# Kernel tuning notes

Measured on AMD Instinct MI355X. Metric: run time of the kernel, lower is better.

Reference implementation:

```python
import jax, jax.numpy as jnp
import numpy as np
import math

HIDDEN = 256
D = 256  # attention_head_size (num_heads=1)
LN_EPS = 1e-5


def setup_inputs() -> dict:
    key = jax.random.key(0)
    ks = jax.random.split(key, 12)
    b, n = 8, 256
    s = 0.02
    return {
        "hidden_states": jax.random.normal(ks[0], (b, n, HIDDEN), jnp.float32),
        "structure_matrix": jax.random.normal(ks[1], (b, n, n, D), jnp.float32),
        "Wq": jax.random.normal(ks[2], (HIDDEN, D), jnp.float32) * s,
        "bq": jnp.zeros((D,), jnp.float32),
        "Wk": jax.random.normal(ks[3], (D, D), jnp.float32) * s,
        "bk": jnp.zeros((D,), jnp.float32),
        "Wv": jax.random.normal(ks[4], (HIDDEN, D), jnp.float32) * s,
        "bv": jnp.zeros((D,), jnp.float32),
        "Wo": jax.random.normal(ks[5], (D, D), jnp.float32) * s,
        "bo": jnp.zeros((D,), jnp.float32),
        "ln_gamma": jnp.ones((D,), jnp.float32),
        "ln_beta": jnp.zeros((D,), jnp.float32),
    }


def _layer_norm(x, gamma, beta):
    mu = jnp.mean(x, axis=-1, keepdims=True)
    var = jnp.mean(jnp.square(x - mu), axis=-1, keepdims=True)
    return (x - mu) * jax.lax.rsqrt(var + LN_EPS) * gamma + beta


def reference(hidden_states, structure_matrix, Wq, bq, Wk, bk, Wv, bv, Wo, bo, ln_gamma, ln_beta):
    # projections
    q = hidden_states @ Wq + bq            # [b, n, d]
    k = structure_matrix @ Wk + bk         # [b, l, r, d]
    v = hidden_states @ Wv + bv            # [b, n, d]
    # pair-biased attention: each (l, r) pair attends over all n tokens
    scores = jnp.einsum('bnd,blrd->blrn', q, k) / math.sqrt(D)  # [b, l, r, n]
    probs = jax.nn.softmax(scores, axis=-1)  # dropout is identity in eval
    ctx = jnp.einsum('blrn,bnd->blrd', probs, v)  # [b, l, r, d]
    out = ctx @ Wo + bo
    return _layer_norm(out + structure_matrix, ln_gamma, ln_beta)
```

## Files before the change

kernel.cpp:

```cpp
#include <hip/hip_runtime.h>
#include <hip/hip_bf16.h>

typedef __attribute__((ext_vector_type(8))) short short8v;
typedef __attribute__((ext_vector_type(4))) float f32x4;
typedef __attribute__((ext_vector_type(8))) unsigned short us8;
typedef const __attribute__((address_space(1))) void* gas_t;
typedef __attribute__((address_space(3))) void* las_t;

__device__ __forceinline__ unsigned short f2bf(float f) {
  union { __hip_bfloat16 h; unsigned short u; } c;
  c.h = __float2bfloat16(f);
  return c.u;
}
__device__ __forceinline__ unsigned int f2bf2(float lo, float hi) {
  union { __hip_bfloat162 h; unsigned int u; } c;
  c.h = __float22bfloat162_rn(make_float2(lo, hi));
  return c.u;
}

__global__ __launch_bounds__(256) void tr_wk(const float* __restrict__ Wk,
                                             float* __restrict__ WkT) {
  __shared__ float sT[64][65];
  const int b = blockIdx.x;
  const int bi = b >> 2, bj = b & 3;
  const int tid = threadIdx.x;
  const int r4 = tid >> 6, c64 = tid & 63;
#pragma unroll
  for (int p = 0; p < 16; p++) {
    const int row = bi * 64 + p * 4 + r4;
    const int col = bj * 64 + c64;
    sT[c64][p * 4 + r4] = Wk[row * 256 + col];
  }
  __syncthreads();
#pragma unroll
  for (int p = 0; p < 16; p++) {
    const int orow = bj * 64 + p * 4 + r4;
    const int ocol = bi * 64 + c64;
    WkT[orow * 256 + ocol] = sT[p * 4 + r4][c64];
  }
}

__global__ __launch_bounds__(256) void make_w(
    const float* __restrict__ WkT, const float* __restrict__ Wq,
    const float* __restrict__ Wv, const float* __restrict__ Wo,
    const float* __restrict__ bq, const float* __restrict__ bk,
    const float* __restrict__ bv, float* __restrict__ WA,
    float* __restrict__ WB, float* __restrict__ wb2,
    float* __restrict__ cq, float* __restrict__ cv, float* __restrict__ cb) {
  __shared__ float wq[256], wv[256], bqs[256], bvs[256];
  const int i = blockIdx.x, t = threadIdx.x;
  wq[t] = Wq[i * 256 + t];
  wv[t] = Wv[i * 256 + t];
  bqs[t] = bq[t];
  bvs[t] = bv[t];
  __syncthreads();
  float sa = 0.f, sb = 0.f;
#pragma unroll 8
  for (int d = 0; d < 256; d++) {
    sa = fmaf(wq[d], WkT[d * 256 + t], sa);
    sb = fmaf(wv[d], Wo[d * 256 + t], sb);
  }
  WA[i * 256 + t] = sa * 0.0625f;
  WB[i * 256 + t] = sb;
  if (t == 0) {
    float s = 0.f;
#pragma unroll 8
    for (int d = 0; d < 256; d++) s = fmaf(wq[d], bk[d], s);
    wb2[i] = s * 0.0625f;
  }
  if (i == 0) {
    float s1 = 0.f, s2 = 0.f;
#pragma unroll 8
    for (int d = 0; d < 256; d++) {
      s1 = fmaf(bqs[d], WkT[d * 256 + t], s1);
      s2 = fmaf(bvs[d], Wo[d * 256 + t], s2);
    }
    cq[t] = s1 * 0.0625f;
    cv[t] = s2;
    if (t == 0) {
      float s = 0.f;
      for (int d = 0; d < 256; d++) s = fmaf(bk[d], bqs[d], s);
      cb[0] = s * 0.0625f;
    }
  }
}

__global__ __launch_bounds__(256) void prep2(
    const float* __restrict__ hs, const float* __restrict__ WA,
    const float* __restrict__ WB, const float* __restrict__ cq,
    const float* __restrict__ cv, const float* __restrict__ wb2,
    const float* __restrict__ cb, unsigned short* __restrict__ W2c,
    unsigned short* __restrict__ V2c, float* __restrict__ bn) {
  __shared__ float rows[8][256];
  __shared__ float w2s[256];
  const int tid = threadIdx.x;
  const int g0 = blockIdx.x * 8;
#pragma unroll
  for (int j = 0; j < 8; j++) rows[j][tid] = hs[(size_t)(g0 + j) * 256 + tid];
  w2s[tid] = wb2[tid];
  __syncthreads();
  const float cqv = cq[tid], cvv = cv[tid];
  float aq[8], av[8];
#pragma unroll
  for (int j = 0; j < 8; j++) { aq[j] = cqv; av[j] = cvv; }
#pragma unroll 8
  for (int i = 0; i < 256; i++) {
    const float wa = WA[i * 256 + tid];
    const float wb = WB[i * 256 + tid];
#pragma unroll
    for (int j = 0; j < 8; j++) {
      aq[j] = fmaf(rows[j][i], wa, aq[j]);
      av[j] = fmaf(rows[j][i], wb, av[j]);
    }
  }
  const int bb = g0 >> 8, n0 = g0 & 255;
  {
    const int kc = tid >> 5, lh = (tid >> 3) & 3, j8 = tid & 7;
    unsigned short* dst = W2c + bb * 65536 + kc * 8192 + (n0 >> 4) * 512 +
                          lh * 128 + (n0 & 15) * 8 + j8;
#pragma unroll
    for (int jj = 0; jj < 8; jj++) dst[jj * 8] = f2bf(aq[jj]);
  }
  {
    const int kc = n0 >> 5, lh = (n0 >> 3) & 3;
    us8 vp;
#pragma unroll
    for (int j = 0; j < 8; j++) vp[j] = f2bf(av[j]);
    *(us8*)(V2c + bb * 65536 + kc * 8192 + (tid >> 4) * 512 + lh * 128 +
            (tid & 15) * 8) = vp;
  }
  if (tid < 8) {
    float s = 0.f;
    for (int i = 0; i < 256; i++) s = fmaf(rows[tid][i], w2s[i], s);
    bn[bb * 256 + n0 + tid] = s + cb[0];
  }
}

__device__ __forceinline__ void stage_b(const unsigned short* src,
                                        unsigned short* lds, int lane) {
#pragma unroll
  for (int i = 0; i < 4; i++)
    __builtin_amdgcn_global_load_lds((gas_t)(src + i * 512 + lane * 8),
                                     (las_t)(lds + i * 512), 16, 0, 0);
}

__global__ __launch_bounds__(256, 3) void pair_attn14(
    const float* __restrict__ S, const float* __restrict__ bo,
    const float* __restrict__ gamma, const float* __restrict__ beta,
    const float* __restrict__ bn, const unsigned short* __restrict__ W2c,
    const unsigned short* __restrict__ V2c, float* __restrict__ out) {
  __shared__ unsigned short sB[3][8192];
  __shared__ float sBn[256];

  const int tid = threadIdx.x;
  const int w = tid >> 6;
  const int lane = tid & 63;
  const int l16 = lane & 15;
  const int lhi = lane >> 4;
  const int bid = blockIdx.x;
  const int idx = (bid & 7) * 1024 + (bid >> 3);
  const int rblk = idx & 3;
  const int lrow = (idx >> 2) & 255;
  const int bat = idx >> 10;

  const size_t base = ((size_t)((bat * 256 + lrow) * 256 + rblk * 64)) * 256;
  const float* Srow = S + base + (size_t)(w * 16 + l16) * 256;

  short8v sf[8];
#pragma unroll
  for (int kc = 0; kc < 8; kc++) {
    const float4 u = *(const float4*)(Srow + kc * 32 + lhi * 8);
    const float4 v = *(const float4*)(Srow + kc * 32 + lhi * 8 + 4);
    us8 p;
    unsigned int* pu = (unsigned int*)&p;
    pu[0] = f2bf2(u.x, u.y);
    pu[1] = f2bf2(u.z, u.w);
    pu[2] = f2bf2(v.x, v.y);
    pu[3] = f2bf2(v.z, v.w);
    sf[kc] = *(short8v*)&p;
  }

  sBn[tid] = bn[bat * 256 + tid];

  asm volatile("s_waitcnt lgkmcnt(0)" ::: "memory");
  asm volatile("s_waitcnt vmcnt(0)" ::: "memory");
  __builtin_amdgcn_sched_barrier(0);

  const unsigned short* W2b = W2c + (size_t)bat * 65536;
  const unsigned short* V2b = V2c + (size_t)bat * 65536;

  stage_b(W2b + 0 * 8192 + w * 2048, &sB[0][w * 2048], lane);
  stage_b(W2b + 1 * 8192 + w * 2048, &sB[1][w * 2048], lane);

  f32x4 acc[16];
  unsigned int pkd[32];
  float psum = 0.f;
#pragma unroll
  for (int t = 0; t < 16; t++) acc[t] = (f32x4){0.f, 0.f, 0.f, 0.f};

  const int A0 = (l16 + ((lhi & 1) * 32)) * 4;
  const int A1 = A0 + 64;
  const bool lo = (lhi < 2);

#pragma unroll
  for (int t = 0; t < 16; t++) {
    if (t < 15) {
      asm volatile("s_waitcnt vmcnt(4)" ::: "memory");
    } else {
      asm volatile("s_waitcnt vmcnt(0)" ::: "memory");
    }
    __builtin_amdgcn_s_barrier();
    if (t + 2 < 16) {
      const int t2 = t + 2;
      const unsigned short* src =
          (t2 < 8) ? (W2b + t2 * 8192) : (V2b + (t2 - 8) * 8192);
      stage_b(src + w * 2048, &sB[t2 % 3][w * 2048], lane);
    }
    __builtin_amdgcn_sched_barrier(0);
    const unsigned short* bbuf = &sB[t % 3][0];

    if (t < 8) {
      __builtin_amdgcn_s_setprio(1);
#pragma unroll
      for (int nt = 0; nt < 16; nt++) {
        const short8v af = *(const short8v*)(bbuf + nt * 512 + lane * 8);
        acc[nt] = __builtin_amdgcn_mfma_f32_16x16x32_bf16(af, sf[t], acc[nt],
                                                          0, 0, 0);
      }
      __builtin_amdgcn_s_setprio(0);
      if (t == 7) {
#pragma unroll
        for (int nt = 0; nt < 16; nt++) {
          const f32x4 b4 = *(const f32x4*)(sBn + nt * 16 + lhi * 4);
          const float p0 = __expf(acc[nt][0] + b4[0]);
          const float p1 = __expf(acc[nt][1] + b4[1]);
          const float p2 = __expf(acc[nt][2] + b4[2]);
          const float p3 = __expf(acc[nt][3] + b4[3]);
          psum += (p0 + p1) + (p2 + p3);
          pkd[nt * 2] = f2bf2(p0, p1);
          pkd[nt * 2 + 1] = f2bf2(p2, p3);
          acc[nt] = (f32x4){0.f, 0.f, 0.f, 0.f};
        }
        psum += __shfl_xor(psum, 16);
        psum += __shfl_xor(psum, 32);
      }
    } else {
      const int qq = t - 8;
      const unsigned int e0 = __builtin_amdgcn_ds_bpermute(A0, pkd[4 * qq + 0]);
      const unsigned int o0 = __builtin_amdgcn_ds_bpermute(A0, pkd[4 * qq + 2]);
      const unsigned int e1 = __builtin_amdgcn_ds_bpermute(A0, pkd[4 * qq + 1]);
      const unsigned int o1 = __builtin_amdgcn_ds_bpermute(A0, pkd[4 * qq + 3]);
      const unsigned int e2 = __builtin_amdgcn_ds_bpermute(A1, pkd[4 * qq + 0]);
      const unsigned int o2 = __builtin_amdgcn_ds_bpermute(A1, pkd[4 * qq + 2]);
      const unsigned int e3 = __builtin_amdgcn_ds_bpermute(A1, pkd[4 * qq + 1]);
      const unsigned int o3 = __builtin_amdgcn_ds_bpermute(A1, pkd[4 * qq + 3]);
      union { unsigned int u[4]; short8v v; } bp_;
      bp_.u[0] = lo ? e0 : o0;
      bp_.u[1] = lo ? e1 : o1;
      bp_.u[2] = lo ? e2 : o2;
      bp_.u[3] = lo ? e3 : o3;
      const short8v bp = bp_.v;
      __builtin_amdgcn_s_setprio(1);
#pragma unroll
      for (int ct = 0; ct < 16; ct++) {
        const short8v af = *(const short8v*)(bbuf + ct * 512 + lane * 8);
        acc[ct] =
            __builtin_amdgcn_mfma_f32_16x16x32_bf16(af, bp, acc[ct], 0, 0, 0);
      }
      __builtin_amdgcn_s_setprio(0);
    }
  }
  __builtin_amdgcn_sched_barrier(0);

  const float inv = 1.f / psum;
  float s1 = 0.f, s2 = 0.f;
#pragma unroll
  for (int ct = 0; ct < 16; ct++) {
    const float4 rz = *(const float4*)(Srow + ct * 16 + lhi * 4);
    const float4 b4 = *(const float4*)(bo + ct * 16 + lhi * 4);
    f32x4 v;
    v[0] = acc[ct][0] * inv + b4.x + rz.x;
    v[1] = acc[ct][1] * inv + b4.y + rz.y;
    v[2] = acc[ct][2] * inv + b4.z + rz.z;
    v[3] = acc[ct][3] * inv + b4.w + rz.w;
#pragma unroll
    for (int g = 0; g < 4; g++) {
      s1 += v[g];
      s2 = fmaf(v[g], v[g], s2);
    }
    acc[ct] = v;
  }
  s1 += __shfl_xor(s1, 16); s2 += __shfl_xor(s2, 16);
  s1 += __shfl_xor(s1, 32); s2 += __shfl_xor(s2, 32);
  const float mean = s1 * (1.f / 256.f);
  const float rstd = rsqrtf(s2 * (1.f / 256.f) - mean * mean + 1e-5f);
  float* Orow = out + base + (size_t)(w * 16 + l16) * 256;
#pragma unroll
  for (int ct = 0; ct < 16; ct++) {
    const float4 g4 = *(const float4*)(gamma + ct * 16 + lhi * 4);
    const float4 be4 = *(const float4*)(beta + ct * 16 + lhi * 4);
    float4 ov;
    ov.x = (acc[ct][0] - mean) * rstd * g4.x + be4.x;
    ov.y = (acc[ct][1] - mean) * rstd * g4.y + be4.y;
    ov.z = (acc[ct][2] - mean) * rstd * g4.z + be4.z;
    ov.w = (acc[ct][3] - mean) * rstd * g4.w + be4.w;
    *(float4*)(Orow + ct * 16 + lhi * 4) = ov;
  }
}

extern "C" void kernel_launch(void* const* d_in, const int* in_sizes, int n_in,
                              void* d_out, int out_size, void* d_ws, size_t ws_size,
                              hipStream_t stream) {
  const float* hs    = (const float*)d_in[0];
  const float* S     = (const float*)d_in[1];
  const float* Wq    = (const float*)d_in[2];
  const float* bq    = (const float*)d_in[3];
  const float* Wk    = (const float*)d_in[4];
  const float* bk    = (const float*)d_in[5];
  const float* Wv    = (const float*)d_in[6];
  const float* bv    = (const float*)d_in[7];
  const float* Wo    = (const float*)d_in[8];
  const float* bo    = (const float*)d_in[9];
  const float* gamma = (const float*)d_in[10];
  const float* beta  = (const float*)d_in[11];

  unsigned short* W2c = (unsigned short*)d_ws;
  unsigned short* V2c = W2c + 8 * 256 * 256;
  float* WA  = (float*)(V2c + 8 * 256 * 256);
  float* WB  = WA + 256 * 256;
  float* WkT = WB + 256 * 256;
  float* wb2 = WkT + 256 * 256;
  float* cq  = wb2 + 256;
  float* cv  = cq + 256;
  float* cb  = cv + 256;
  float* bnp = cb + 256;

  tr_wk<<<16, 256, 0, stream>>>(Wk, WkT);
  make_w<<<256, 256, 0, stream>>>(WkT, Wq, Wv, Wo, bq, bk, bv, WA, WB, wb2,
                                  cq, cv, cb);
  prep2<<<256, 256, 0, stream>>>(hs, WA, WB, cq, cv, wb2, cb, W2c, V2c, bnp);
  pair_attn14<<<8192, 256, 0, stream>>>(S, bo, gamma, beta, bnp, W2c, V2c,
                                        (float*)d_out);
}
```

Before: 513.2 us.

## Switch pair attention MFMAs from bf16 to fp8 with a deeper LDS pipeline

Converts the structure-matrix fragments, the precomputed W2/V2 operands and the softmax probabilities to fp8 and uses fp8 MFMA instructions. W2 is scaled by 256 and the scores are rescaled before the exponent. This halves LDS staging bytes, allows a 4-deep buffer ring with 3-ahead prefetch, and raises the occupancy hint to 4 blocks. The aim is to cut MFMA and LDS cost, at the risk of lower numerical accuracy from fp8 rounding of the inputs and probabilities.

Measured after the change: 526.6 us. 2.6% more time.

```diff
diff --git a/kernel.cpp b/kernel.cpp
--- a/kernel.cpp
+++ b/kernel.cpp
@@ -1,21 +1,25 @@
 #include <hip/hip_runtime.h>
 #include <hip/hip_bf16.h>
 
-typedef __attribute__((ext_vector_type(8))) short short8v;
 typedef __attribute__((ext_vector_type(4))) float f32x4;
-typedef __attribute__((ext_vector_type(8))) unsigned short us8;
+typedef __attribute__((ext_vector_type(2))) long long ll2;
 typedef const __attribute__((address_space(1))) void* gas_t;
 typedef __attribute__((address_space(3))) void* las_t;
 
-__device__ __forceinline__ unsigned short f2bf(float f) {
-  union { __hip_bfloat16 h; unsigned short u; } c;
-  c.h = __float2bfloat16(f);
-  return c.u;
-}
-__device__ __forceinline__ unsigned int f2bf2(float lo, float hi) {
-  union { __hip_bfloat162 h; unsigned int u; } c;
-  c.h = __float22bfloat162_rn(make_float2(lo, hi));
-  return c.u;
+__device__ __forceinline__ unsigned int pk4f8(float a, float b, float c,
+                                              float d) {
+  unsigned int r = 0;
+  r = (unsigned int)__builtin_amdgcn_cvt_pk_fp8_f32(a, b, (int)r, false);
+  r = (unsigned int)__builtin_amdgcn_cvt_pk_fp8_f32(c, d, (int)r, true);
+  return r;
+}
+__device__ __forceinline__ unsigned char f8(float x) {
+  return (unsigned char)(__builtin_amdgcn_cvt_pk_fp8_f32(x, 0.f, 0, false) &
+                         0xff);
+}
+__device__ __forceinline__ long long mk64(unsigned int lo, unsigned int hi) {
+  return (long long)((unsigned long long)lo |
+                     ((unsigned long long)hi << 32));
 }
 
 __global__ __launch_bounds__(256) void tr_wk(const float* __restrict__ Wk,
@@ -26,18 +30,12 @@
   const int tid = threadIdx.x;
   const int r4 = tid >> 6, c64 = tid & 63;
 #pragma unroll
-  for (int p = 0; p < 16; p++) {
-    const int row = bi * 64 + p * 4 + r4;
-    const int col = bj * 64 + c64;
-    sT[c64][p * 4 + r4] = Wk[row * 256 + col];
-  }
+  for (int p = 0; p < 16; p++)
+    sT[c64][p * 4 + r4] = Wk[(bi * 64 + p * 4 + r4) * 256 + bj * 64 + c64];
   __syncthreads();
 #pragma unroll
-  for (int p = 0; p < 16; p++) {
-    const int orow = bj * 64 + p * 4 + r4;
-    const int ocol = bi * 64 + c64;
-    WkT[orow * 256 + ocol] = sT[p * 4 + r4][c64];
-  }
+  for (int p = 0; p < 16; p++)
+    WkT[(bj * 64 + p * 4 + r4) * 256 + bi * 64 + c64] = sT[p * 4 + r4][c64];
 }
 
 __global__ __launch_bounds__(256) void make_w(
@@ -89,8 +87,8 @@
     const float* __restrict__ hs, const float* __restrict__ WA,
     const float* __restrict__ WB, const float* __restrict__ cq,
     const float* __restrict__ cv, const float* __restrict__ wb2,
-    const float* __restrict__ cb, unsigned short* __restrict__ W2c,
-    unsigned short* __restrict__ V2c, float* __restrict__ bn) {
+    const float* __restrict__ cb, unsigned char* __restrict__ W2c,
+    unsigned char* __restrict__ V2c, float* __restrict__ bn) {
   __shared__ float rows[8][256];
   __shared__ float w2s[256];
   const int tid = threadIdx.x;
@@ -115,19 +113,21 @@
   }
   const int bb = g0 >> 8, n0 = g0 & 255;
   {
-    const int kc = tid >> 5, lh = (tid >> 3) & 3, j8 = tid & 7;
-    unsigned short* dst = W2c + bb * 65536 + kc * 8192 + (n0 >> 4) * 512 +
-                          lh * 128 + (n0 & 15) * 8 + j8;
-#pragma unroll
-    for (int jj = 0; jj < 8; jj++) dst[jj * 8] = f2bf(aq[jj]);
+    unsigned char* dst = W2c + bb * 65536 + (tid >> 5) * 8192 +
+                         (n0 >> 5) * 1024 + ((tid >> 3) & 3) * 256 +
+                         ((n0 >> 4) & 1) * 8 + (tid & 7);
+#pragma unroll
+    for (int jj = 0; jj < 8; jj++)
+      dst[((n0 & 15) + jj) * 16] = f8(aq[jj] * 256.f);
   }
   {
-    const int kc = n0 >> 5, lh = (n0 >> 3) & 3;
-    us8 vp;
-#pragma unroll
-    for (int j = 0; j < 8; j++) vp[j] = f2bf(av[j]);
-    *(us8*)(V2c + bb * 65536 + kc * 8192 + (tid >> 4) * 512 + lh * 128 +
-            (tid & 15) * 8) = vp;
+    unsigned char* dst = V2c + bb * 65536 + (n0 >> 5) * 8192 +
+                         (tid >> 5) * 1024 + ((n0 >> 3) & 3) * 256 +
+                         (tid & 15) * 16 + ((tid >> 4) & 1) * 8;
+    const unsigned int lo = pk4f8(av[0], av[1], av[2], av[3]);
+    const unsigned int hi = pk4f8(av[4], av[5], av[6], av[7]);
+    *(unsigned long long*)dst =
+        (unsigned long long)lo | ((unsigned long long)hi << 32);
   }
   if (tid < 8) {
     float s = 0.f;
@@ -136,20 +136,20 @@
   }
 }
 
-__device__ __forceinline__ void stage_b(const unsigned short* src,
-                                        unsigned short* lds, int lane) {
-#pragma unroll
-  for (int i = 0; i < 4; i++)
-    __builtin_amdgcn_global_load_lds((gas_t)(src + i * 512 + lane * 8),
-                                     (las_t)(lds + i * 512), 16, 0, 0);
-}
-
-__global__ __launch_bounds__(256, 3) void pair_attn14(
+__device__ __forceinline__ void stage_b(const unsigned char* src,
+                                        unsigned char* lds, int lane) {
+#pragma unroll
+  for (int i = 0; i < 2; i++)
+    __builtin_amdgcn_global_load_lds((gas_t)(src + i * 1024 + lane * 16),
+                                     (las_t)(lds + i * 1024), 16, 0, 0);
+}
+
+__global__ __launch_bounds__(256, 4) void pair_attn15(
     const float* __restrict__ S, const float* __restrict__ bo,
     const float* __restrict__ gamma, const float* __restrict__ beta,
-    const float* __restrict__ bn, const unsigned short* __restrict__ W2c,
-    const unsigned short* __restrict__ V2c, float* __restrict__ out) {
-  __shared__ unsigned short sB[3][8192];
+    const float* __restrict__ bn, const unsigned char* __restrict__ W2c,
+    const unsigned char* __restrict__ V2c, float* __restrict__ out) {
+  __shared__ unsigned char sB[4][8192];
   __shared__ float sBn[256];
 
   const int tid = threadIdx.x;
@@ -166,18 +166,12 @@
   const size_t base = ((size_t)((bat * 256 + lrow) * 256 + rblk * 64)) * 256;
   const float* Srow = S + base + (size_t)(w * 16 + l16) * 256;
 
-  short8v sf[8];
+  long long sf[8];
 #pragma unroll
   for (int kc = 0; kc < 8; kc++) {
     const float4 u = *(const float4*)(Srow + kc * 32 + lhi * 8);
     const float4 v = *(const float4*)(Srow + kc * 32 + lhi * 8 + 4);
-    us8 p;
-    unsigned int* pu = (unsigned int*)&p;
-    pu[0] = f2bf2(u.x, u.y);
-    pu[1] = f2bf2(u.z, u.w);
-    pu[2] = f2bf2(v.x, v.y);
-    pu[3] = f2bf2(v.z, v.w);
-    sf[kc] = *(short8v*)&p;
+    sf[kc] = mk64(pk4f8(u.x, u.y, u.z, u.w), pk4f8(v.x, v.y, v.z, v.w));
   }
 
   sBn[tid] = bn[bat * 256 + tid];
@@ -186,59 +180,63 @@
   asm volatile("s_waitcnt vmcnt(0)" ::: "memory");
   __builtin_amdgcn_sched_barrier(0);
 
-  const unsigned short* W2b = W2c + (size_t)bat * 65536;
-  const unsigned short* V2b = V2c + (size_t)bat * 65536;
+  const unsigned char* W2b = W2c + (size_t)bat * 65536;
+  const unsigned char* V2b = V2c + (size_t)bat * 65536;
 
   stage_b(W2b + 0 * 8192 + w * 2048, &sB[0][w * 2048], lane);
   stage_b(W2b + 1 * 8192 + w * 2048, &sB[1][w * 2048], lane);
+  stage_b(W2b + 2 * 8192 + w * 2048, &sB[2][w * 2048], lane);
 
   f32x4 acc[16];
-  unsigned int pkd[32];
+  unsigned int pkd[16];
   float psum = 0.f;
 #pragma unroll
   for (int t = 0; t < 16; t++) acc[t] = (f32x4){0.f, 0.f, 0.f, 0.f};
 
-  const int A0 = (l16 + ((lhi & 1) * 32)) * 4;
+  const int A0 = (((lhi & 1) * 2) * 16 + l16) * 4;
   const int A1 = A0 + 64;
-  const bool lo = (lhi < 2);
+  const bool hsel = (lhi >> 1) != 0;
 
 #pragma unroll
   for (int t = 0; t < 16; t++) {
-    if (t < 15) {
+    if (t < 14) {
       asm volatile("s_waitcnt vmcnt(4)" ::: "memory");
+    } else if (t == 14) {
+      asm volatile("s_waitcnt vmcnt(2)" ::: "memory");
     } else {
       asm volatile("s_waitcnt vmcnt(0)" ::: "memory");
     }
     __builtin_amdgcn_s_barrier();
-    if (t + 2 < 16) {
-      const int t2 = t + 2;
-      const unsigned short* src =
-          (t2 < 8) ? (W2b + t2 * 8192) : (V2b + (t2 - 8) * 8192);
-      stage_b(src + w * 2048, &sB[t2 % 3][w * 2048], lane);
+    if (t + 3 < 16) {
+      const int t3 = t + 3;
+      const unsigned char* src =
+          (t3 < 8) ? (W2b + t3 * 8192) : (V2b + (t3 - 8) * 8192);
+      stage_b(src + w * 2048, &sB[t3 & 3][w * 2048], lane);
     }
     __builtin_amdgcn_sched_barrier(0);
-    const unsigned short* bbuf = &sB[t % 3][0];
+    const unsigned char* bbuf = &sB[t & 3][0];
 
     if (t < 8) {
       __builtin_amdgcn_s_setprio(1);
 #pragma unroll
-      for (int nt = 0; nt < 16; nt++) {
-        const short8v af = *(const short8v*)(bbuf + nt * 512 + lane * 8);
-        acc[nt] = __builtin_amdgcn_mfma_f32_16x16x32_bf16(af, sf[t], acc[nt],
-                                                          0, 0, 0);
+      for (int p = 0; p < 8; p++) {
+        const ll2 ap = *(const ll2*)(bbuf + p * 1024 + lane * 16);
+        acc[2 * p] = __builtin_amdgcn_mfma_f32_16x16x32_fp8_fp8(
+            ap[0], sf[t], acc[2 * p], 0, 0, 0);
+        acc[2 * p + 1] = __builtin_amdgcn_mfma_f32_16x16x32_fp8_fp8(
+            ap[1], sf[t], acc[2 * p + 1], 0, 0, 0);
       }
       __builtin_amdgcn_s_setprio(0);
       if (t == 7) {
 #pragma unroll
         for (int nt = 0; nt < 16; nt++) {
           const f32x4 b4 = *(const f32x4*)(sBn + nt * 16 + lhi * 4);
-          const float p0 = __expf(acc[nt][0] + b4[0]);
-          const float p1 = __expf(acc[nt][1] + b4[1]);
-          const float p2 = __expf(acc[nt][2] + b4[2]);
-          const float p3 = __expf(acc[nt][3] + b4[3]);
+          const float p0 = __expf(fmaf(acc[nt][0], 0.00390625f, b4[0]));
+          const float p1 = __expf(fmaf(acc[nt][1], 0.00390625f, b4[1]));
+          const float p2 = __expf(fmaf(acc[nt][2], 0.00390625f, b4[2]));
+          const float p3 = __expf(fmaf(acc[nt][3], 0.00390625f, b4[3]));
           psum += (p0 + p1) + (p2 + p3);
-          pkd[nt * 2] = f2bf2(p0, p1);
-          pkd[nt * 2 + 1] = f2bf2(p2, p3);
+          pkd[nt] = pk4f8(p0, p1, p2, p3);
           acc[nt] = (f32x4){0.f, 0.f, 0.f, 0.f};
         }
         psum += __shfl_xor(psum, 16);
@@ -246,26 +244,21 @@
       }
     } else {
       const int qq = t - 8;
-      const unsigned int e0 = __builtin_amdgcn_ds_bpermute(A0, pkd[4 * qq + 0]);
-      const unsigned int o0 = __builtin_amdgcn_ds_bpermute(A0, pkd[4 * qq + 2]);
-      const unsigned int e1 = __builtin_amdgcn_ds_bpermute(A0, pkd[4 * qq + 1]);
-      const unsigned int o1 = __builtin_amdgcn_ds_bpermute(A0, pkd[4 * qq + 3]);
-      const unsigned int e2 = __builtin_amdgcn_ds_bpermute(A1, pkd[4 * qq + 0]);
-      const unsigned int o2 = __builtin_amdgcn_ds_bpermute(A1, pkd[4 * qq + 2]);
-      const unsigned int e3 = __builtin_amdgcn_ds_bpermute(A1, pkd[4 * qq + 1]);
-      const unsigned int o3 = __builtin_amdgcn_ds_bpermute(A1, pkd[4 * qq + 3]);
-      union { unsigned int u[4]; short8v v; } bp_;
-      bp_.u[0] = lo ? e0 : o0;
-      bp_.u[1] = lo ? e1 : o1;
-      bp_.u[2] = lo ? e2 : o2;
-      bp_.u[3] = lo ? e3 : o3;
-      const short8v bp = bp_.v;
+      const unsigned int e0 = __builtin_amdgcn_ds_bpermute(A0, pkd[2 * qq]);
+      const unsigned int e1 = __builtin_amdgcn_ds_bpermute(A1, pkd[2 * qq]);
+      const unsigned int f0 =
+          __builtin_amdgcn_ds_bpermute(A0, pkd[2 * qq + 1]);
+      const unsigned int f1 =
+          __builtin_amdgcn_ds_bpermute(A1, pkd[2 * qq + 1]);
+      const long long bp = mk64(hsel ? f0 : e0, hsel ? f1 : e1);
       __builtin_amdgcn_s_setprio(1);
 #pragma unroll
-      for (int ct = 0; ct < 16; ct++) {
-        const short8v af = *(const short8v*)(bbuf + ct * 512 + lane * 8);
-        acc[ct] =
-            __builtin_amdgcn_mfma_f32_16x16x32_bf16(af, bp, acc[ct], 0, 0, 0);
+      for (int p = 0; p < 8; p++) {
+        const ll2 ap = *(const ll2*)(bbuf + p * 1024 + lane * 16);
+        acc[2 * p] = __builtin_amdgcn_mfma_f32_16x16x32_fp8_fp8(
+            ap[0], bp, acc[2 * p], 0, 0, 0);
+        acc[2 * p + 1] = __builtin_amdgcn_mfma_f32_16x16x32_fp8_fp8(
+            ap[1], bp, acc[2 * p + 1], 0, 0, 0);
       }
       __builtin_amdgcn_s_setprio(0);
     }
@@ -324,9 +317,9 @@
   const float* gamma = (const float*)d_in[10];
   const float* beta  = (const float*)d_in[11];
 
-  unsigned short* W2c = (unsigned short*)d_ws;
-  unsigned short* V2c = W2c + 8 * 256 * 256;
-  float* WA  = (float*)(V2c + 8 * 256 * 256);
+  unsigned char* W2c = (unsigned char*)d_ws;
+  unsigned char* V2c = W2c + 8 * 65536;
+  float* WA  = (float*)(V2c + 8 * 65536);
   float* WB  = WA + 256 * 256;
   float* WkT = WB + 256 * 256;
   float* wb2 = WkT + 256 * 256;
@@ -339,6 +332,6 @@
   make_w<<<256, 256, 0, stream>>>(WkT, Wq, Wv, Wo, bq, bk, bv, WA, WB, wb2,
                                   cq, cv, cb);
   prep2<<<256, 256, 0, stream>>>(hs, WA, WB, cq, cv, wb2, cb, W2c, V2c, bnp);
-  pair_attn14<<<8192, 256, 0, stream>>>(S, bo, gamma, beta, bnp, W2c, V2c,
+  pair_attn15<<<8192, 256, 0, stream>>>(S, bo, gamma, beta, bnp, W2c, V2c,
                                         (float*)d_out);
 }
```
